# Kernel tuning notes

Hardware: AMD Instinct MI355X
Metric: run time of the kernel (lower is better)

The kernel has to match this reference:

```python
import jax, jax.numpy as jnp
import numpy as np

B, T, D = 8, 1024, 512
H = 8
F_OUT = D // H          # 64 per head
ALPHA = 0.2             # LeakyReLU slope in GAT
MASK_RATE = 0.3
GAMMA = 0.0625          # DistanceAdj gamma
BIAS = 0.2              # DistanceAdj bias
LN_EPS = 1e-5
NEG_INF = -9e15
L2_EPS = 1e-12          # F.normalize eps


def setup_inputs() -> dict:
    key = jax.random.key(0)
    ks = jax.random.split(key, 8)
    return {
        "x": jax.random.normal(ks[0], (B, T, D), jnp.float32),
        "W": jax.random.normal(ks[1], (H, D, F_OUT), jnp.float32) * 0.05,
        "a_src": jax.random.normal(ks[2], (H, F_OUT), jnp.float32) * 0.05,
        "a_dst": jax.random.normal(ks[3], (H, F_OUT), jnp.float32) * 0.05,
        "W2": jax.random.normal(ks[4], (D, D), jnp.float32) * 0.02,
        "b2": jnp.zeros((D,), jnp.float32),
        "ln_g": jnp.ones((D,), jnp.float32),
        "ln_b": jnp.zeros((D,), jnp.float32),
    }


def _distance_adj(batch, t):
    # DistanceAdj: Gaussian kernel over temporal index distance, shared across batch
    idx = jnp.arange(t, dtype=jnp.float32)
    d2 = (idx[:, None] - idx[None, :]) ** 2
    adj = jnp.exp(-GAMMA * d2 - BIAS)                      # [T, T]
    return jnp.broadcast_to(adj[None], (batch, t, t))      # [B, T, T]


def reference(x, W, a_src, a_dst, W2, b2, ln_g, ln_b):
    b, t, d = x.shape
    adj = _distance_adj(b, t)

    # top-k magnitude node selection -> row/col union mask (index_fill loop)
    k = int(MASK_RATE * t)
    mags = jnp.linalg.norm(x, axis=2)                      # [B, T]
    _, topk = jax.lax.top_k(mags, k)                       # [B, k]
    sel = jnp.zeros((b, t), bool).at[jnp.arange(b)[:, None], topk].set(True)
    mask = sel[:, :, None] | sel[:, None, :]               # rows OR cols filled
    adj = jnp.where(mask, adj, 0.0)

    # GAT multi-head attention (dense masked form, dropout=0 at eval)
    Wh = jnp.einsum("btd,hdf->bhtf", x, W)                 # [B,H,T,F']
    e_src = jnp.einsum("bhtf,hf->bht", Wh, a_src)
    e_dst = jnp.einsum("bhtf,hf->bht", Wh, a_dst)
    e = jax.nn.leaky_relu(e_src[..., :, None] + e_dst[..., None, :], ALPHA)
    e = jnp.where(adj[:, None] > 0, e, NEG_INF)            # masked logits
    attn = jax.nn.softmax(e, axis=-1)                      # [B,H,T,T]
    hp = jnp.einsum("bhts,bhsf->bhtf", attn, Wh)
    hp = jax.nn.elu(hp)                                    # concat=True -> elu per head
    tmp = hp.transpose(0, 2, 1, 3).reshape(b, t, d)        # concat heads -> [B,T,512]

    # signed-sqrt + F.normalize (default dim=1 -> over T axis)
    tmp = jnp.sqrt(jax.nn.relu(tmp)) - jnp.sqrt(jax.nn.relu(-tmp))
    nrm = jnp.linalg.norm(tmp, axis=1, keepdims=True)      # [B,1,D]
    tmp = tmp / jnp.maximum(nrm, L2_EPS)

    # residual linear + LayerNorm + permute
    y = x + tmp @ W2 + b2
    mu = jnp.mean(y, axis=-1, keepdims=True)
    var = jnp.mean((y - mu) ** 2, axis=-1, keepdims=True)
    y = (y - mu) / jnp.sqrt(var + LN_EPS) * ln_g + ln_b
    return y.transpose(0, 2, 1)                            # [B, D, T]
```

## Files before the change

### kernel.cpp

```cpp
#include <hip/hip_runtime.h>
#include <hip/hip_bf16.h>

typedef unsigned short u16;
typedef short bf16x8 __attribute__((ext_vector_type(8)));
typedef float f32x4 __attribute__((ext_vector_type(4)));
typedef int   i32x4 __attribute__((ext_vector_type(4)));

#define NB 8
#define NT 1024
#define ND 512
#define KSEL 307
#define PSTR 152
#define TSTR 136

__device__ __forceinline__ float bf2f(u16 u){
  union { unsigned int i; float f; } c; c.i = ((unsigned int)u) << 16; return c.f;
}
__device__ __forceinline__ u16 f2bf(float f){
  __hip_bfloat16 h = __float2bfloat16(f);
  u16 u; __builtin_memcpy(&u, &h, 2); return u;
}

__global__ void k_select(const float* __restrict__ mags, int* __restrict__ sel){
  __shared__ float sm[NT];
  int b = blockIdx.x;
  int tid = threadIdx.x;
  for (int i = tid; i < NT; i += 256) sm[i] = mags[b * NT + i];
  __syncthreads();
  int tl = tid >> 2, tq = tid & 3;
  int t = blockIdx.y * 64 + tl;
  float m = sm[t];
  int cnt = 0;
  int s0 = tq * 256;
  for (int s = s0; s < s0 + 256; s++){
    float v = sm[s];
    cnt += (v > m) || (v == m && s < t);
  }
  cnt += __shfl_xor(cnt, 1, 64);
  cnt += __shfl_xor(cnt, 2, 64);
  if (tq == 0) sel[b * NT + t] = (cnt < KSEL) ? 1 : 0;
}

__launch_bounds__(256, 3)
__global__ void k_gemm_wh(const float* __restrict__ x, const float* __restrict__ Wf,
                          const float* __restrict__ a_src, const float* __restrict__ a_dst,
                          u16* __restrict__ WhT, float* __restrict__ es, float* __restrict__ ed,
                          float* __restrict__ mags, float* __restrict__ cn,
                          float* __restrict__ rz){
  __shared__ u16 smem[8704];
  u16* As = smem;
  u16* Bs = smem + 5120;
  int m0 = blockIdx.x * 128;
  int h  = blockIdx.y;
  int tid = threadIdx.x;
  if (h == 0 && tid < 64) cn[blockIdx.x * 64 + tid] = 0.f;
  if (h == 1) rz[blockIdx.x * 256 + tid] = 0.f;
  int wv = tid >> 6, lane = tid & 63;
  int quad = lane >> 4, lr = lane & 15;
  f32x4 acc[2][4] = {};
  float sq[2] = {0.f, 0.f};
  int ar = (tid * 8) >> 5, ac = (tid * 8) & 31;
  const float* xa0 = &x[(size_t)(m0 + ar) * 512 + ac];
  const float* xa1 = xa0 + (size_t)64 * 512;
  int kk = (tid * 8) >> 6, f0 = (tid * 8) & 63;
  const float* wb = &Wf[((size_t)h << 15) + (size_t)kk * 64 + f0];
  int bbase = f0 * 40 + (((kk >> 3) ^ ((f0 >> 3) & 3)) * 8) + (kk & 7);
  f32x4 pa0 = *(const f32x4*)xa0, pa1 = *(const f32x4*)(xa0 + 4);
  f32x4 pa2 = *(const f32x4*)xa1, pa3 = *(const f32x4*)(xa1 + 4);
  f32x4 pb0 = *(const f32x4*)wb,  pb1 = *(const f32x4*)(wb + 4);
  for (int kt = 0; kt < 512; kt += 32){
    __syncthreads();
    {
      u16 pk[8];
      if (h == 0){
#pragma unroll
        for (int q = 0; q < 4; q++) sq[0] += pa0[q]*pa0[q] + pa1[q]*pa1[q];
#pragma unroll
        for (int q = 0; q < 4; q++) sq[1] += pa2[q]*pa2[q] + pa3[q]*pa3[q];
      }
#pragma unroll
      for (int q = 0; q < 4; q++){ pk[q] = f2bf(pa0[q]); pk[4+q] = f2bf(pa1[q]); }
      *(bf16x8*)&As[ar*40 + ac] = *(const bf16x8*)pk;
#pragma unroll
      for (int q = 0; q < 4; q++){ pk[q] = f2bf(pa2[q]); pk[4+q] = f2bf(pa3[q]); }
      *(bf16x8*)&As[(ar + 64)*40 + ac] = *(const bf16x8*)pk;
#pragma unroll
      for (int q = 0; q < 4; q++) Bs[bbase + q*40]       = f2bf(pb0[q]);
#pragma unroll
      for (int q = 0; q < 4; q++) Bs[bbase + (q+4)*40]   = f2bf(pb1[q]);
    }
    __syncthreads();
    if (kt < 480){
      pa0 = *(const f32x4*)(xa0 + kt + 32); pa1 = *(const f32x4*)(xa0 + kt + 36);
      pa2 = *(const f32x4*)(xa1 + kt + 32); pa3 = *(const f32x4*)(xa1 + kt + 36);
      pb0 = *(const f32x4*)(wb + (size_t)(kt + 32) * 64);
      pb1 = *(const f32x4*)(wb + (size_t)(kt + 32) * 64 + 4);
    }
    bf16x8 af[2], bfr[4];
#pragma unroll
    for (int i = 0; i < 2; i++) af[i] = *(const bf16x8*)&As[(wv*32 + i*16 + lr)*40 + quad*8];
#pragma unroll
    for (int i = 0; i < 4; i++){
      int f = i*16 + lr;
      bfr[i] = *(const bf16x8*)&Bs[f*40 + ((quad ^ ((f >> 3) & 3)) * 8)];
    }
#pragma unroll
    for (int mi = 0; mi < 2; mi++)
#pragma unroll
      for (int ni = 0; ni < 4; ni++)
        acc[mi][ni] = __builtin_amdgcn_mfma_f32_16x16x32_bf16(af[mi], bfr[ni], acc[mi][ni], 0, 0, 0);
  }
  if (h == 0){
#pragma unroll
    for (int i = 0; i < 2; i++){
      float s = sq[i];
      s += __shfl_xor(s, 1, 64);
      s += __shfl_xor(s, 2, 64);
      if ((tid & 3) == 0) mags[m0 + i*64 + (tid >> 2)] = sqrtf(s);
    }
  }
  float asv[4], adv[4];
#pragma unroll
  for (int ni = 0; ni < 4; ni++){
    asv[ni] = a_src[h*64 + ni*16 + lr];
    adv[ni] = a_dst[h*64 + ni*16 + lr];
  }
#pragma unroll
  for (int mi = 0; mi < 2; mi++)
#pragma unroll
    for (int r = 0; r < 4; r++){
      float pes = 0.f, ped = 0.f;
#pragma unroll
      for (int ni = 0; ni < 4; ni++){
        pes += acc[mi][ni][r] * asv[ni];
        ped += acc[mi][ni][r] * adv[ni];
      }
#pragma unroll
      for (int mofs = 1; mofs < 16; mofs <<= 1){
        pes += __shfl_xor(pes, mofs, 64);
        ped += __shfl_xor(ped, mofs, 64);
      }
      if (lr == 0){
        int rowg = m0 + wv*32 + mi*16 + quad*4 + r;
        int bb_ = rowg >> 10, tt = rowg & 1023;
        es[(bb_ * 8 + h) * NT + tt] = pes;
        ed[(bb_ * 8 + h) * NT + tt] = ped;
      }
    }
  __syncthreads();
  u16* Tr = smem;
#pragma unroll
  for (int mi = 0; mi < 2; mi++)
#pragma unroll
    for (int ni = 0; ni < 4; ni++){
      int fl = ni*16 + lr;
      int tl = wv*32 + mi*16 + quad*4;
#pragma unroll
      for (int r = 0; r < 4; r++) Tr[fl*TSTR + tl + r] = f2bf(acc[mi][ni][r]);
    }
  __syncthreads();
  int f = tid >> 2, seg = tid & 3;
  int b_ = m0 >> 10;
  u16* dst = &WhT[(b_ * 512 + h * 64 + f) * NT + (m0 & 1023) + seg*32];
  const u16* srcp = &Tr[f*TSTR + seg*32];
#pragma unroll
  for (int k8 = 0; k8 < 4; k8++)
    *(bf16x8*)(dst + k8*8) = *(const bf16x8*)(srcp + k8*8);
}

__launch_bounds__(256)
__global__ void k_attn(const u16* __restrict__ WhT, const float* __restrict__ es,
                       const float* __restrict__ ed, const int* __restrict__ sel,
                       u16* __restrict__ t2b, float* __restrict__ cn){
  __shared__ u16 P[64 * PSTR];
  __shared__ float edw[144];
  __shared__ int   selw[144];
  __shared__ float esw[64];
  __shared__ float swv[64];
  int bh = blockIdx.x;
  int b = bh >> 3;
  int t0 = blockIdx.y * 64;
  int tid = threadIdx.x;
  int wv = tid >> 6, lane = tid & 63;
  int quad = lane >> 4, lr = lane & 15;
  int s_base = t0 - 40;
  for (int i = tid; i < 144; i += 256){
    int s = s_base + i;
    bool ok = (s >= 0 && s < NT);
    edw[i]  = ok ? ed[bh * NT + s] : 0.f;
    selw[i] = ok ? sel[b * NT + s] : 0;
  }
  if (tid < 64) esw[tid] = es[bh * NT + t0 + tid];
  {
    i32x4 z = {};
    for (int i = lane; i < 304; i += 64){
      int r16 = i / 19, c16 = i - r16 * 19;
      *(i32x4*)&P[(16*wv + r16) * PSTR + c16 * 8] = z;
    }
  }
  __syncthreads();
  {
    int tl = 16*wv + (lane >> 2);
    int q = lane & 3;
    float e_t = esw[tl];
    int sel_t = selw[tl + 40];
    float part = 0.f;
    for (int j = q; j <= 80; j += 4){
      int sw = tl + j;
      int s = s_base + sw;
      float w = 0.f;
      if (s >= 0 && s < NT && (sel_t | selw[sw])){
        float v = e_t + edw[sw];
        v = v > 0.f ? v : 0.2f * v;
        v = fminf(v, 60.f);
        w = bf2f(f2bf(__expf(v)));
      }
      part += w;
      if (w != 0.f) P[tl * PSTR + sw] = f2bf(w);
    }
    part += __shfl_xor(part, 1, 64);
    part += __shfl_xor(part, 2, 64);
    if (q == 0) swv[tl] = part;
  }
  f32x4 acc[4] = {};
  const u16* vbase = WhT + (bh * 64) * NT;
#pragma unroll
  for (int ks = 0; ks < 96; ks += 32){
    bf16x8 afr = *(const bf16x8*)&P[(16*wv + lr) * PSTR + 16*wv + ks + quad*8];
    int tb = s_base + 16*wv + ks + quad*8;
    bool ok = (tb >= 0) && (tb < NT);
    bf16x8 zf = {};
#pragma unroll
    for (int jn = 0; jn < 4; jn++){
      bf16x8 bfr = ok ? *(const bf16x8*)&vbase[(16*jn + lr) * NT + tb] : zf;
      acc[jn] = __builtin_amdgcn_mfma_f32_16x16x32_bf16(afr, bfr, acc[jn], 0, 0, 0);
    }
  }
#pragma unroll
  for (int jn = 0; jn < 4; jn++){
    float ssum = 0.f;
#pragma unroll
    for (int r = 0; r < 4; r++){
      int t_loc = 16*wv + quad*4 + r;
      float sw_ = swv[t_loc];
      float hp = acc[jn][r] / (sw_ > 0.f ? sw_ : 1.f);
      hp = hp > 0.f ? hp : (__expf(hp) - 1.f);
      float o = hp >= 0.f ? sqrtf(hp) : -sqrtf(-hp);
      ssum += o * o;
      t2b[(b * NT + t0 + t_loc) * ND + (bh & 7) * 64 + 16*jn + lr] = f2bf(o);
    }
    ssum += __shfl_xor(ssum, 16, 64);
    ssum += __shfl_xor(ssum, 32, 64);
    if (quad == 0) atomicAdd(&cn[b * ND + (bh & 7) * 64 + 16*jn + lr], ssum);
  }
}

__launch_bounds__(256, 3)
__global__ void k_gemm2(const u16* __restrict__ A, const float* __restrict__ W2f,
                        const float* __restrict__ xres, const float* __restrict__ b2,
                        const float* __restrict__ cn, float* __restrict__ Y,
                        float* __restrict__ rsum, float* __restrict__ rqsum){
  __shared__ u16 As[128 * 40];
  __shared__ u16 Bs[64 * 40];
  __shared__ float scl[512];
  int m0 = blockIdx.x * 128, n0 = blockIdx.y * 64;
  int tid = threadIdx.x;
  int wv = tid >> 6, lane = tid & 63;
  int quad = lane >> 4, lr = lane & 15;
  int bb0 = (m0 >> 10) << 9;
  for (int i = tid; i < 512; i += 256){
    float nv = sqrtf(cn[bb0 + i]);
    scl[i] = 1.f / fmaxf(nv, 1e-12f);
  }
  f32x4 acc[2][4] = {};
  int ar = (tid * 8) >> 5, ac = (tid * 8) & 31;
  const u16* ap0 = &A[(size_t)(m0 + ar) * 512 + ac];
  const u16* ap1 = ap0 + (size_t)64 * 512;
  int kk = (tid * 8) >> 6, j0 = (tid * 8) & 63;
  const float* w2b = &W2f[(size_t)kk * 512 + n0 + j0];
  int bbase = j0 * 40 + (((kk >> 3) ^ ((j0 >> 3) & 3)) * 8) + (kk & 7);
  bf16x8 ra0 = *(const bf16x8*)ap0;
  bf16x8 ra1 = *(const bf16x8*)ap1;
  f32x4 pb0 = *(const f32x4*)w2b, pb1 = *(const f32x4*)(w2b + 4);
  for (int kt = 0; kt < 512; kt += 32){
    __syncthreads();
    {
      u16 pk0[8], pk1[8];
#pragma unroll
      for (int q = 0; q < 8; q++){
        float sv = scl[kt + ac + q];
        pk0[q] = f2bf(bf2f((u16)ra0[q]) * sv);
        pk1[q] = f2bf(bf2f((u16)ra1[q]) * sv);
      }
      *(bf16x8*)&As[ar*40 + ac]        = *(const bf16x8*)pk0;
      *(bf16x8*)&As[(ar + 64)*40 + ac] = *(const bf16x8*)pk1;
#pragma unroll
      for (int q = 0; q < 4; q++) Bs[bbase + q*40]     = f2bf(pb0[q]);
#pragma unroll
      for (int q = 0; q < 4; q++) Bs[bbase + (q+4)*40] = f2bf(pb1[q]);
    }
    __syncthreads();
    if (kt < 480){
      ra0 = *(const bf16x8*)(ap0 + kt + 32);
      ra1 = *(const bf16x8*)(ap1 + kt + 32);
      pb0 = *(const f32x4*)(w2b + (size_t)(kt + 32) * 512);
      pb1 = *(const f32x4*)(w2b + (size_t)(kt + 32) * 512 + 4);
    }
    bf16x8 af[2], bfr[4];
#pragma unroll
    for (int i = 0; i < 2; i++) af[i] = *(const bf16x8*)&As[(wv*32 + i*16 + lr)*40 + quad*8];
#pragma unroll
    for (int i = 0; i < 4; i++){
      int f = i*16 + lr;
      bfr[i] = *(const bf16x8*)&Bs[f*40 + ((quad ^ ((f >> 3) & 3)) * 8)];
    }
#pragma unroll
    for (int mi = 0; mi < 2; mi++)
#pragma unroll
      for (int ni = 0; ni < 4; ni++)
        acc[mi][ni] = __builtin_amdgcn_mfma_f32_16x16x32_bf16(af[mi], bfr[ni], acc[mi][ni], 0, 0, 0);
  }
  float b2v[4];
#pragma unroll
  for (int ni = 0; ni < 4; ni++) b2v[ni] = b2[n0 + ni*16 + lr];
#pragma unroll
  for (int mi = 0; mi < 2; mi++){
    int rgb = m0 + wv*32 + mi*16 + quad*4;
#pragma unroll
    for (int r = 0; r < 4; r++){
      int row = rgb + r;
      float rs = 0.f, rq = 0.f;
#pragma unroll
      for (int ni = 0; ni < 4; ni++){
        int cg = n0 + ni*16 + lr;
        int idx = row * 512 + cg;
        float yv = acc[mi][ni][r] + xres[idx] + b2v[ni];
        Y[idx] = yv;
        rs += yv; rq += yv * yv;
      }
#pragma unroll
      for (int m2 = 1; m2 < 16; m2 <<= 1){
        rs += __shfl_xor(rs, m2, 64);
        rq += __shfl_xor(rq, m2, 64);
      }
      if (lr == 0){
        atomicAdd(&rsum[row], rs);
        atomicAdd(&rqsum[row], rq);
      }
    }
  }
}

__global__ void k_outln(const float* __restrict__ Y, const float* __restrict__ rsum,
                        const float* __restrict__ rqsum, const float* __restrict__ g,
                        const float* __restrict__ bb, float* __restrict__ out){
  __shared__ float mus[64], rss[64];
  __shared__ float tile[64 * 65];
  int t0 = blockIdx.x * 64, b = blockIdx.y;
  int cbase = blockIdx.z * 128;
  int tid = threadIdx.x;
  if (tid < 64){
    int row = b * NT + t0 + tid;
    float m = rsum[row] * (1.f/512.f);
    float var = rqsum[row] * (1.f/512.f) - m * m;
    mus[tid] = m;
    rss[tid] = 1.f / sqrtf(var + 1e-5f);
  }
  __syncthreads();
  int j = tid & 63, i0 = tid >> 6;
  for (int c0 = cbase; c0 < cbase + 128; c0 += 64){
#pragma unroll
    for (int k = 0; k < 16; k++){
      int i = i0 + k * 4;
      float v = (Y[(b * NT + t0 + i) * ND + c0 + j] - mus[i]) * rss[i] * g[c0 + j] + bb[c0 + j];
      tile[i * 65 + j] = v;
    }
    __syncthreads();
#pragma unroll
    for (int k = 0; k < 16; k++){
      int jj = i0 + k * 4;
      out[(b * ND + c0 + jj) * NT + t0 + j] = tile[j * 65 + jj];
    }
    __syncthreads();
  }
}

extern "C" void kernel_launch(void* const* d_in, const int* in_sizes, int n_in,
                              void* d_out, int out_size, void* d_ws, size_t ws_size,
                              hipStream_t stream) {
  (void)in_sizes; (void)n_in; (void)out_size; (void)ws_size;
  const float* x     = (const float*)d_in[0];
  const float* W     = (const float*)d_in[1];
  const float* a_src = (const float*)d_in[2];
  const float* a_dst = (const float*)d_in[3];
  const float* W2    = (const float*)d_in[4];
  const float* b2    = (const float*)d_in[5];
  const float* ln_g  = (const float*)d_in[6];
  const float* ln_b  = (const float*)d_in[7];
  char* ws = (char*)d_ws;
  int*   sel   = (int*)  (ws + 256);
  float* mags  = (float*)(ws + 33024);
  float* es    = (float*)(ws + 1124608);
  float* ed    = (float*)(ws + 1386752);
  float* cn    = (float*)(ws + 1648896);
  float* rsum  = (float*)(ws + 1665280);
  float* rqsum = (float*)(ws + 1698048);
  u16*   WhT   = (u16*)  (ws + 2097152);
  u16*   t2b   = (u16*)  (ws + 18874368);
  float* Y     = (float*)(ws + 2097152);
  float* out   = (float*)d_out;

  k_gemm_wh  <<<dim3(64, 8), 256, 0, stream>>>(x, W, a_src, a_dst, WhT, es, ed, mags, cn, rsum);
  k_select   <<<dim3(NB, 16), 256, 0, stream>>>(mags, sel);
  k_attn     <<<dim3(64, 16), 256, 0, stream>>>(WhT, es, ed, sel, t2b, cn);
  k_gemm2    <<<dim3(64, 8), 256, 0, stream>>>(t2b, W2, x, b2, cn, Y, rsum, rqsum);
  k_outln    <<<dim3(16, NB, 4), 256, 0, stream>>>(Y, rsum, rqsum, ln_g, ln_b, out);
}
```

Before: 147.5 us.

## Fuse five kernels into one cooperative persistent kernel with grid syncs

Merges gemm_wh, select, attention, gemm2 and layernorm-transpose into a single cooperative kernel of 512 blocks, separated by grid.sync barriers. Each phase is a device function working in one shared-memory buffer, and each block runs two attention tiles. The goal is to remove four kernel launch gaps and their tail effects. The cost is that every grid barrier stalls all blocks. Occupancy is also capped at 2 blocks per CU and shared memory is sized to the largest phase.

```diff
diff --git a/kernel.cpp b/kernel.cpp
--- a/kernel.cpp
+++ b/kernel.cpp
@@ -1,5 +1,8 @@
 #include <hip/hip_runtime.h>
 #include <hip/hip_bf16.h>
+#include <hip/hip_cooperative_groups.h>
+
+namespace cg = cooperative_groups;
 
 typedef unsigned short u16;
 typedef short bf16x8 __attribute__((ext_vector_type(8)));
@@ -21,40 +24,17 @@
   u16 u; __builtin_memcpy(&u, &h, 2); return u;
 }
 
-__global__ void k_select(const float* __restrict__ mags, int* __restrict__ sel){
-  __shared__ float sm[NT];
-  int b = blockIdx.x;
-  int tid = threadIdx.x;
-  for (int i = tid; i < NT; i += 256) sm[i] = mags[b * NT + i];
-  __syncthreads();
-  int tl = tid >> 2, tq = tid & 3;
-  int t = blockIdx.y * 64 + tl;
-  float m = sm[t];
-  int cnt = 0;
-  int s0 = tq * 256;
-  for (int s = s0; s < s0 + 256; s++){
-    float v = sm[s];
-    cnt += (v > m) || (v == m && s < t);
-  }
-  cnt += __shfl_xor(cnt, 1, 64);
-  cnt += __shfl_xor(cnt, 2, 64);
-  if (tq == 0) sel[b * NT + t] = (cnt < KSEL) ? 1 : 0;
-}
-
-__launch_bounds__(256, 3)
-__global__ void k_gemm_wh(const float* __restrict__ x, const float* __restrict__ Wf,
-                          const float* __restrict__ a_src, const float* __restrict__ a_dst,
-                          u16* __restrict__ WhT, float* __restrict__ es, float* __restrict__ ed,
-                          float* __restrict__ mags, float* __restrict__ cn,
-                          float* __restrict__ rz){
-  __shared__ u16 smem[8704];
+__device__ __forceinline__ void phase_gemm_wh(char* smraw, int mb, int h, int tid,
+    const float* __restrict__ x, const float* __restrict__ Wf,
+    const float* __restrict__ a_src, const float* __restrict__ a_dst,
+    u16* __restrict__ WhT, float* __restrict__ es, float* __restrict__ ed,
+    float* __restrict__ mags, float* __restrict__ cn, float* __restrict__ rz){
+  u16* smem = (u16*)smraw;
   u16* As = smem;
   u16* Bs = smem + 5120;
-  int m0 = blockIdx.x * 128;
-  int h  = blockIdx.y;
-  int tid = threadIdx.x;
-  if (h == 0 && tid < 64) cn[blockIdx.x * 64 + tid] = 0.f;
-  if (h == 1) rz[blockIdx.x * 256 + tid] = 0.f;
+  int m0 = mb * 128;
+  if (h == 0 && tid < 64) cn[mb * 64 + tid] = 0.f;
+  if (h == 1) rz[mb * 256 + tid] = 0.f;
   int wv = tid >> 6, lane = tid & 63;
   int quad = lane >> 4, lr = lane & 15;
   f32x4 acc[2][4] = {};
@@ -168,22 +148,39 @@
     *(bf16x8*)(dst + k8*8) = *(const bf16x8*)(srcp + k8*8);
 }
 
-__launch_bounds__(256)
-__global__ void k_attn(const u16* __restrict__ WhT, const float* __restrict__ es,
-                       const float* __restrict__ ed, const int* __restrict__ sel,
-                       u16* __restrict__ t2b, float* __restrict__ cn){
-  __shared__ u16 P[64 * PSTR];
-  __shared__ float edw[144];
-  __shared__ int   selw[144];
-  __shared__ float esw[64];
-  __shared__ float swv[64];
-  int bh = blockIdx.x;
+__device__ __forceinline__ void phase_select(char* smraw, int b, int by, int tid,
+    const float* __restrict__ mags, int* __restrict__ sel){
+  float* sm = (float*)smraw;
+  for (int i = tid; i < NT; i += 256) sm[i] = mags[b * NT + i];
+  __syncthreads();
+  int tl = tid >> 2, tq = tid & 3;
+  int t = by * 64 + tl;
+  float m = sm[t];
+  int cnt = 0;
+  int s0 = tq * 256;
+  for (int s = s0; s < s0 + 256; s++){
+    float v = sm[s];
+    cnt += (v > m) || (v == m && s < t);
+  }
+  cnt += __shfl_xor(cnt, 1, 64);
+  cnt += __shfl_xor(cnt, 2, 64);
+  if (tq == 0) sel[b * NT + t] = (cnt < KSEL) ? 1 : 0;
+}
+
+__device__ __forceinline__ void phase_attn(char* smraw, int bh, int ty, int tid,
+    const u16* __restrict__ WhT, const float* __restrict__ es, const float* __restrict__ ed,
+    const int* __restrict__ sel, u16* __restrict__ t2b, float* __restrict__ cn){
+  u16*   P    = (u16*)smraw;
+  float* edw  = (float*)(smraw + 19456);
+  int*   selw = (int*)  (smraw + 20032);
+  float* esw  = (float*)(smraw + 20608);
+  float* swv  = (float*)(smraw + 20864);
   int b = bh >> 3;
-  int t0 = blockIdx.y * 64;
-  int tid = threadIdx.x;
+  int t0 = ty * 64;
   int wv = tid >> 6, lane = tid & 63;
   int quad = lane >> 4, lr = lane & 15;
   int s_base = t0 - 40;
+  __syncthreads();
   for (int i = tid; i < 144; i += 256){
     int s = s_base + i;
     bool ok = (s >= 0 && s < NT);
@@ -222,6 +219,7 @@
     part += __shfl_xor(part, 2, 64);
     if (q == 0) swv[tl] = part;
   }
+  __syncthreads();
   f32x4 acc[4] = {};
   const u16* vbase = WhT + (bh * 64) * NT;
 #pragma unroll
@@ -255,19 +253,19 @@
   }
 }
 
-__launch_bounds__(256, 3)
-__global__ void k_gemm2(const u16* __restrict__ A, const float* __restrict__ W2f,
-                        const float* __restrict__ xres, const float* __restrict__ b2,
-                        const float* __restrict__ cn, float* __restrict__ Y,
-                        float* __restrict__ rsum, float* __restrict__ rqsum){
-  __shared__ u16 As[128 * 40];
-  __shared__ u16 Bs[64 * 40];
-  __shared__ float scl[512];
-  int m0 = blockIdx.x * 128, n0 = blockIdx.y * 64;
-  int tid = threadIdx.x;
+__device__ __forceinline__ void phase_gemm2(char* smraw, int mb, int nb, int tid,
+    const u16* __restrict__ A, const float* __restrict__ W2f,
+    const float* __restrict__ xres, const float* __restrict__ b2,
+    const float* __restrict__ cn, float* __restrict__ Y,
+    float* __restrict__ rsum, float* __restrict__ rqsum){
+  u16*   As  = (u16*)smraw;
+  u16*   Bs  = (u16*)(smraw + 10240);
+  float* scl = (float*)(smraw + 15360);
+  int m0 = mb * 128, n0 = nb * 64;
   int wv = tid >> 6, lane = tid & 63;
   int quad = lane >> 4, lr = lane & 15;
   int bb0 = (m0 >> 10) << 9;
+  __syncthreads();
   for (int i = tid; i < 512; i += 256){
     float nv = sqrtf(cn[bb0 + i]);
     scl[i] = 1.f / fmaxf(nv, 1e-12f);
@@ -351,14 +349,16 @@
   }
 }
 
-__global__ void k_outln(const float* __restrict__ Y, const float* __restrict__ rsum,
-                        const float* __restrict__ rqsum, const float* __restrict__ g,
-                        const float* __restrict__ bb, float* __restrict__ out){
-  __shared__ float mus[64], rss[64];
-  __shared__ float tile[64 * 65];
-  int t0 = blockIdx.x * 64, b = blockIdx.y;
-  int cbase = blockIdx.z * 128;
-  int tid = threadIdx.x;
+__device__ __forceinline__ void phase_outln(char* smraw, int xb, int b, int zb, int tid,
+    const float* __restrict__ Y, const float* __restrict__ rsum,
+    const float* __restrict__ rqsum, const float* __restrict__ g,
+    const float* __restrict__ bb, float* __restrict__ out){
+  float* mus  = (float*)smraw;
+  float* rss  = (float*)(smraw + 256);
+  float* tile = (float*)(smraw + 512);
+  int t0 = xb * 64;
+  int cbase = zb * 128;
+  __syncthreads();
   if (tid < 64){
     int row = b * NT + t0 + tid;
     float m = rsum[row] * (1.f/512.f);
@@ -383,6 +383,30 @@
     }
     __syncthreads();
   }
+}
+
+__global__ void __launch_bounds__(256, 2)
+k_mega(const float* __restrict__ x, const float* __restrict__ Wf,
+       const float* __restrict__ a_src, const float* __restrict__ a_dst,
+       const float* __restrict__ W2f, const float* __restrict__ b2,
+       const float* __restrict__ ln_g, const float* __restrict__ ln_b,
+       u16* __restrict__ WhT, float* __restrict__ es, float* __restrict__ ed,
+       float* __restrict__ mags, int* __restrict__ sel, float* __restrict__ cn,
+       float* __restrict__ rsum, float* __restrict__ rqsum, u16* __restrict__ t2b,
+       float* __restrict__ Y, float* __restrict__ out){
+  __shared__ __align__(16) char smraw[21184];
+  cg::grid_group grid = cg::this_grid();
+  int bid = blockIdx.x, tid = threadIdx.x;
+  phase_gemm_wh(smraw, bid & 63, bid >> 6, tid, x, Wf, a_src, a_dst, WhT, es, ed, mags, cn, rsum);
+  grid.sync();
+  if (bid < 128) phase_select(smraw, bid >> 4, bid & 15, tid, mags, sel);
+  grid.sync();
+  phase_attn(smraw, bid & 63, bid >> 6,       tid, WhT, es, ed, sel, t2b, cn);
+  phase_attn(smraw, bid & 63, 8 + (bid >> 6), tid, WhT, es, ed, sel, t2b, cn);
+  grid.sync();
+  phase_gemm2(smraw, bid & 63, bid >> 6, tid, t2b, W2f, x, b2, cn, Y, rsum, rqsum);
+  grid.sync();
+  phase_outln(smraw, bid & 15, (bid >> 4) & 7, bid >> 7, tid, Y, rsum, rqsum, ln_g, ln_b, out);
 }
 
 extern "C" void kernel_launch(void* const* d_in, const int* in_sizes, int n_in,
@@ -410,9 +434,11 @@
   float* Y     = (float*)(ws + 2097152);
   float* out   = (float*)d_out;
 
-  k_gemm_wh  <<<dim3(64, 8), 256, 0, stream>>>(x, W, a_src, a_dst, WhT, es, ed, mags, cn, rsum);
-  k_select   <<<dim3(NB, 16), 256, 0, stream>>>(mags, sel);
-  k_attn     <<<dim3(64, 16), 256, 0, stream>>>(WhT, es, ed, sel, t2b, cn);
-  k_gemm2    <<<dim3(64, 8), 256, 0, stream>>>(t2b, W2, x, b2, cn, Y, rsum, rqsum);
-  k_outln    <<<dim3(16, NB, 4), 256, 0, stream>>>(Y, rsum, rqsum, ln_g, ln_b, out);
-}
+  void* args[] = {
+    (void*)&x, (void*)&W, (void*)&a_src, (void*)&a_dst, (void*)&W2, (void*)&b2,
+    (void*)&ln_g, (void*)&ln_b, (void*)&WhT, (void*)&es, (void*)&ed, (void*)&mags,
+    (void*)&sel, (void*)&cn, (void*)&rsum, (void*)&rqsum, (void*)&t2b, (void*)&Y,
+    (void*)&out
+  };
+  hipLaunchCooperativeKernel((const void*)k_mega, dim3(512), dim3(256), args, 0, stream);
+}
```

New measurement: 399.7 us. +171.0%, slower.

## Fuse output GEMM with LayerNorm and transpose; pre-transpose W2 to bf16

Applied to the files above, without the earlier changes.

The second GEMM and the LayerNorm/transpose kernel are merged into one kernel. Each 512-thread block computes full 32-row strips across all 512 columns, so row statistics are reduced in shared memory instead of through global atomics, and the fp32 Y intermediate round-trip is gone. W2 is transposed and converted to bf16 once inside the first GEMM kernel, using blocks with h==2, so the fused kernel can load B tiles directly as bf16 vectors. There are fewer blocks (256), each using large shared memory, which may lower occupancy. Each block also reloads the whole W2 for every strip. A __syncthreads is also added in the attention kernel.

```diff
diff --git a/kernel.cpp b/kernel.cpp
--- a/kernel.cpp
+++ b/kernel.cpp
@@ -43,10 +43,11 @@
 
 __launch_bounds__(256, 3)
 __global__ void k_gemm_wh(const float* __restrict__ x, const float* __restrict__ Wf,
+                          const float* __restrict__ W2f,
                           const float* __restrict__ a_src, const float* __restrict__ a_dst,
                           u16* __restrict__ WhT, float* __restrict__ es, float* __restrict__ ed,
                           float* __restrict__ mags, float* __restrict__ cn,
-                          float* __restrict__ rz){
+                          u16* __restrict__ W2T){
   __shared__ u16 smem[8704];
   u16* As = smem;
   u16* Bs = smem + 5120;
@@ -54,7 +55,21 @@
   int h  = blockIdx.y;
   int tid = threadIdx.x;
   if (h == 0 && tid < 64) cn[blockIdx.x * 64 + tid] = 0.f;
-  if (h == 1) rz[blockIdx.x * 256 + tid] = 0.f;
+  if (h == 2){
+    float* tile = (float*)smem;
+    int kt0 = (blockIdx.x >> 3) * 64, n00 = (blockIdx.x & 7) * 64;
+    int r = tid >> 6, cl = tid & 63;
+#pragma unroll
+    for (int p = 0; p < 16; p++)
+      tile[(r + p*4)*65 + cl] = W2f[(size_t)(kt0 + r + p*4) * 512 + n00 + cl];
+    __syncthreads();
+#pragma unroll
+    for (int p = 0; p < 16; p++){
+      int orow = r + p*4;
+      W2T[(size_t)(n00 + orow) * 512 + kt0 + cl] = f2bf(tile[cl*65 + orow]);
+    }
+    __syncthreads();
+  }
   int wv = tid >> 6, lane = tid & 63;
   int quad = lane >> 4, lr = lane & 15;
   f32x4 acc[2][4] = {};
@@ -222,6 +237,7 @@
     part += __shfl_xor(part, 2, 64);
     if (q == 0) swv[tl] = part;
   }
+  __syncthreads();
   f32x4 acc[4] = {};
   const u16* vbase = WhT + (bh * 64) * NT;
 #pragma unroll
@@ -255,65 +271,62 @@
   }
 }
 
-__launch_bounds__(256, 3)
-__global__ void k_gemm2(const u16* __restrict__ A, const float* __restrict__ W2f,
-                        const float* __restrict__ xres, const float* __restrict__ b2,
-                        const float* __restrict__ cn, float* __restrict__ Y,
-                        float* __restrict__ rsum, float* __restrict__ rqsum){
-  __shared__ u16 As[128 * 40];
-  __shared__ u16 Bs[64 * 40];
-  __shared__ float scl[512];
-  int m0 = blockIdx.x * 128, n0 = blockIdx.y * 64;
+__launch_bounds__(512)
+__global__ void k_gemm2ln(const u16* __restrict__ A, const u16* __restrict__ W2T,
+                          const float* __restrict__ xres, const float* __restrict__ b2,
+                          const float* __restrict__ cn, const float* __restrict__ g,
+                          const float* __restrict__ bb, float* __restrict__ out){
+  __shared__ __align__(16) char smraw[69888];
+  u16*   As  = (u16*)smraw;
+  u16*   Bs  = (u16*)(smraw + 2560);
+  float* scl = (float*)(smraw + 43520);
+  float* T     = (float*)smraw;
+  float* wpart = (float*)(smraw + 67584);
+  float* mus   = (float*)(smraw + 69632);
+  float* rss   = (float*)(smraw + 69760);
   int tid = threadIdx.x;
-  int wv = tid >> 6, lane = tid & 63;
+  int m0 = blockIdx.x * 32;
+  int b  = m0 >> 10, t0 = m0 & 1023;
+  int w = tid >> 6, lane = tid & 63;
   int quad = lane >> 4, lr = lane & 15;
-  int bb0 = (m0 >> 10) << 9;
-  for (int i = tid; i < 512; i += 256){
-    float nv = sqrtf(cn[bb0 + i]);
-    scl[i] = 1.f / fmaxf(nv, 1e-12f);
-  }
+  {
+    float nv = sqrtf(cn[(b << 9) + tid]);
+    scl[tid] = 1.f / fmaxf(nv, 1e-12f);
+  }
+  int ar = tid >> 2, ac = (tid & 3) * 8;
+  const u16* ap = &A[(size_t)(m0 + ar) * 512 + ac];
+  int nb_ = tid >> 2, c = (tid & 3) * 8;
+  bf16x8 ra = {}, rb[4];
+  if (tid < 128) ra = *(const bf16x8*)ap;
+#pragma unroll
+  for (int rep = 0; rep < 4; rep++)
+    rb[rep] = *(const bf16x8*)&W2T[(size_t)(nb_ + rep*128) * 512 + c];
   f32x4 acc[2][4] = {};
-  int ar = (tid * 8) >> 5, ac = (tid * 8) & 31;
-  const u16* ap0 = &A[(size_t)(m0 + ar) * 512 + ac];
-  const u16* ap1 = ap0 + (size_t)64 * 512;
-  int kk = (tid * 8) >> 6, j0 = (tid * 8) & 63;
-  const float* w2b = &W2f[(size_t)kk * 512 + n0 + j0];
-  int bbase = j0 * 40 + (((kk >> 3) ^ ((j0 >> 3) & 3)) * 8) + (kk & 7);
-  bf16x8 ra0 = *(const bf16x8*)ap0;
-  bf16x8 ra1 = *(const bf16x8*)ap1;
-  f32x4 pb0 = *(const f32x4*)w2b, pb1 = *(const f32x4*)(w2b + 4);
   for (int kt = 0; kt < 512; kt += 32){
     __syncthreads();
-    {
-      u16 pk0[8], pk1[8];
-#pragma unroll
-      for (int q = 0; q < 8; q++){
-        float sv = scl[kt + ac + q];
-        pk0[q] = f2bf(bf2f((u16)ra0[q]) * sv);
-        pk1[q] = f2bf(bf2f((u16)ra1[q]) * sv);
-      }
-      *(bf16x8*)&As[ar*40 + ac]        = *(const bf16x8*)pk0;
-      *(bf16x8*)&As[(ar + 64)*40 + ac] = *(const bf16x8*)pk1;
-#pragma unroll
-      for (int q = 0; q < 4; q++) Bs[bbase + q*40]     = f2bf(pb0[q]);
-#pragma unroll
-      for (int q = 0; q < 4; q++) Bs[bbase + (q+4)*40] = f2bf(pb1[q]);
-    }
+    if (tid < 128){
+      u16 pk[8];
+#pragma unroll
+      for (int q = 0; q < 8; q++)
+        pk[q] = f2bf(bf2f((u16)ra[q]) * scl[kt + ac + q]);
+      *(bf16x8*)&As[ar*40 + ac] = *(const bf16x8*)pk;
+    }
+#pragma unroll
+    for (int rep = 0; rep < 4; rep++)
+      *(bf16x8*)&Bs[(nb_ + rep*128)*40 + c] = rb[rep];
     __syncthreads();
     if (kt < 480){
-      ra0 = *(const bf16x8*)(ap0 + kt + 32);
-      ra1 = *(const bf16x8*)(ap1 + kt + 32);
-      pb0 = *(const f32x4*)(w2b + (size_t)(kt + 32) * 512);
-      pb1 = *(const f32x4*)(w2b + (size_t)(kt + 32) * 512 + 4);
+      if (tid < 128) ra = *(const bf16x8*)(ap + kt + 32);
+#pragma unroll
+      for (int rep = 0; rep < 4; rep++)
+        rb[rep] = *(const bf16x8*)&W2T[(size_t)(nb_ + rep*128) * 512 + kt + 32 + c];
     }
     bf16x8 af[2], bfr[4];
 #pragma unroll
-    for (int i = 0; i < 2; i++) af[i] = *(const bf16x8*)&As[(wv*32 + i*16 + lr)*40 + quad*8];
-#pragma unroll
-    for (int i = 0; i < 4; i++){
-      int f = i*16 + lr;
-      bfr[i] = *(const bf16x8*)&Bs[f*40 + ((quad ^ ((f >> 3) & 3)) * 8)];
-    }
+    for (int mi = 0; mi < 2; mi++) af[mi] = *(const bf16x8*)&As[(mi*16 + lr)*40 + quad*8];
+#pragma unroll
+    for (int i = 0; i < 4; i++)
+      bfr[i] = *(const bf16x8*)&Bs[(w*64 + i*16 + lr)*40 + quad*8];
 #pragma unroll
     for (int mi = 0; mi < 2; mi++)
 #pragma unroll
@@ -322,21 +335,20 @@
   }
   float b2v[4];
 #pragma unroll
-  for (int ni = 0; ni < 4; ni++) b2v[ni] = b2[n0 + ni*16 + lr];
-#pragma unroll
-  for (int mi = 0; mi < 2; mi++){
-    int rgb = m0 + wv*32 + mi*16 + quad*4;
+  for (int ni = 0; ni < 4; ni++) b2v[ni] = b2[w*64 + ni*16 + lr];
+  float yv[2][4][4];
+#pragma unroll
+  for (int mi = 0; mi < 2; mi++)
 #pragma unroll
     for (int r = 0; r < 4; r++){
-      int row = rgb + r;
+      int rl = mi*16 + quad*4 + r;
       float rs = 0.f, rq = 0.f;
 #pragma unroll
       for (int ni = 0; ni < 4; ni++){
-        int cg = n0 + ni*16 + lr;
-        int idx = row * 512 + cg;
-        float yv = acc[mi][ni][r] + xres[idx] + b2v[ni];
-        Y[idx] = yv;
-        rs += yv; rq += yv * yv;
+        int col = w*64 + ni*16 + lr;
+        float v = acc[mi][ni][r] + xres[(size_t)(m0 + rl) * 512 + col] + b2v[ni];
+        yv[mi][ni][r] = v;
+        rs += v; rq += v * v;
       }
 #pragma unroll
       for (int m2 = 1; m2 < 16; m2 <<= 1){
@@ -344,44 +356,48 @@
         rq += __shfl_xor(rq, m2, 64);
       }
       if (lr == 0){
-        atomicAdd(&rsum[row], rs);
-        atomicAdd(&rqsum[row], rq);
-      }
-    }
-  }
-}
-
-__global__ void k_outln(const float* __restrict__ Y, const float* __restrict__ rsum,
-                        const float* __restrict__ rqsum, const float* __restrict__ g,
-                        const float* __restrict__ bb, float* __restrict__ out){
-  __shared__ float mus[64], rss[64];
-  __shared__ float tile[64 * 65];
-  int t0 = blockIdx.x * 64, b = blockIdx.y;
-  int cbase = blockIdx.z * 128;
-  int tid = threadIdx.x;
-  if (tid < 64){
-    int row = b * NT + t0 + tid;
-    float m = rsum[row] * (1.f/512.f);
-    float var = rqsum[row] * (1.f/512.f) - m * m;
-    mus[tid] = m;
+        wpart[w*32 + rl]       = rs;
+        wpart[256 + w*32 + rl] = rq;
+      }
+    }
+  __syncthreads();
+  if (tid < 32){
+    float s = 0.f, q = 0.f;
+#pragma unroll
+    for (int wv2 = 0; wv2 < 8; wv2++){
+      s += wpart[wv2*32 + tid];
+      q += wpart[256 + wv2*32 + tid];
+    }
+    float mu = s * (1.f/512.f);
+    float var = q * (1.f/512.f) - mu * mu;
+    mus[tid] = mu;
     rss[tid] = 1.f / sqrtf(var + 1e-5f);
   }
   __syncthreads();
-  int j = tid & 63, i0 = tid >> 6;
-  for (int c0 = cbase; c0 < cbase + 128; c0 += 64){
-#pragma unroll
-    for (int k = 0; k < 16; k++){
-      int i = i0 + k * 4;
-      float v = (Y[(b * NT + t0 + i) * ND + c0 + j] - mus[i]) * rss[i] * g[c0 + j] + bb[c0 + j];
-      tile[i * 65 + j] = v;
-    }
-    __syncthreads();
-#pragma unroll
-    for (int k = 0; k < 16; k++){
-      int jj = i0 + k * 4;
-      out[(b * ND + c0 + jj) * NT + t0 + j] = tile[j * 65 + jj];
-    }
-    __syncthreads();
+  float gv[4], bv[4];
+#pragma unroll
+  for (int ni = 0; ni < 4; ni++){
+    gv[ni] = g[w*64 + ni*16 + lr];
+    bv[ni] = bb[w*64 + ni*16 + lr];
+  }
+#pragma unroll
+  for (int mi = 0; mi < 2; mi++)
+#pragma unroll
+    for (int r = 0; r < 4; r++){
+      int rl = mi*16 + quad*4 + r;
+      float mu = mus[rl], rstd = rss[rl];
+#pragma unroll
+      for (int ni = 0; ni < 4; ni++){
+        int col = w*64 + ni*16 + lr;
+        T[col*33 + rl] = (yv[mi][ni][r] - mu) * rstd * gv[ni] + bv[ni];
+      }
+    }
+  __syncthreads();
+  int j = tid & 31, dq = tid >> 5;
+#pragma unroll
+  for (int kk2 = 0; kk2 < 32; kk2++){
+    int d = dq + kk2 * 16;
+    out[((size_t)(b * 512 + d)) * 1024 + t0 + j] = T[d*33 + j];
   }
 }
 
@@ -403,16 +419,13 @@
   float* es    = (float*)(ws + 1124608);
   float* ed    = (float*)(ws + 1386752);
   float* cn    = (float*)(ws + 1648896);
-  float* rsum  = (float*)(ws + 1665280);
-  float* rqsum = (float*)(ws + 1698048);
   u16*   WhT   = (u16*)  (ws + 2097152);
   u16*   t2b   = (u16*)  (ws + 18874368);
-  float* Y     = (float*)(ws + 2097152);
+  u16*   W2T   = (u16*)  (ws + 36175872);
   float* out   = (float*)d_out;
 
-  k_gemm_wh  <<<dim3(64, 8), 256, 0, stream>>>(x, W, a_src, a_dst, WhT, es, ed, mags, cn, rsum);
+  k_gemm_wh  <<<dim3(64, 8), 256, 0, stream>>>(x, W, W2, a_src, a_dst, WhT, es, ed, mags, cn, W2T);
   k_select   <<<dim3(NB, 16), 256, 0, stream>>>(mags, sel);
   k_attn     <<<dim3(64, 16), 256, 0, stream>>>(WhT, es, ed, sel, t2b, cn);
-  k_gemm2    <<<dim3(64, 8), 256, 0, stream>>>(t2b, W2, x, b2, cn, Y, rsum, rqsum);
-  k_outln    <<<dim3(16, NB, 4), 256, 0, stream>>>(Y, rsum, rqsum, ln_g, ln_b, out);
-}
+  k_gemm2ln  <<<dim3(256), 512, 0, stream>>>(t2b, W2T, x, b2, cn, ln_g, ln_b, out);
+}
```

Result: faster. 143.7 us (-2.6%).
